# Optimization experiments

Hardware: AMD Instinct MI355X
Metric: run time of the kernel (lower is better)

## Reference

```python
import jax, jax.numpy as jnp
import numpy as np

B, S, F = 512, 512, 128   # batch, seq_len, facts_size (= querry_size)
H1, H2 = 80, 40
PAD = float(-2**32 + 1)


def setup_inputs() -> dict:
    key = jax.random.key(0)
    ks = jax.random.split(key, 12)
    inp = {
        "query": jax.random.normal(ks[0], (B, F), jnp.float32),
        "facts": jax.random.normal(ks[1], (B, S, F), jnp.float32),
        "mask": jax.random.randint(ks[2], (B, S), 0, 2, jnp.int32),
        # mlp1: querry_size -> facts_size
        "W1": jax.random.normal(ks[3], (F, F), jnp.float32) / np.sqrt(F),
        "b1": jnp.zeros((F,), jnp.float32),
        # PReLU alpha (per-feature, init zeros)
        "alpha": jnp.zeros((F,), jnp.float32),
        # mlp2: 4*F -> 80
        "W2": jax.random.normal(ks[4], (4 * F, H1), jnp.float32) / np.sqrt(4 * F),
        "b2": jnp.zeros((H1,), jnp.float32),
        # mlp3: 80 -> 40
        "W3": jax.random.normal(ks[5], (H1, H2), jnp.float32) / np.sqrt(H1),
        "b3": jnp.zeros((H2,), jnp.float32),
        # mlp4: 40 -> 1
        "W4": jax.random.normal(ks[6], (H2, 1), jnp.float32) / np.sqrt(H2),
        "b4": jnp.zeros((1,), jnp.float32),
    }
    return inp


def reference(query, facts, mask, W1, b1, alpha, W2, b2, W3, b3, W4, b4):
    # mlp1 + PReLU on the query
    q = query @ W1 + b1                                   # [B, F]
    q = jnp.where(q >= 0, q, alpha * q)                   # PReLU, alpha per-feature
    # broadcast query over sequence (tile+reshape in the original)
    qs = jnp.broadcast_to(q[:, None, :], (q.shape[0], S, F))  # [B, S, F]
    din = jnp.concatenate([qs, facts, qs - facts, qs * facts], axis=-1)  # [B,S,4F]
    h1 = jax.nn.sigmoid(din @ W2 + b2)                    # [B, S, 80]
    h2 = jax.nn.sigmoid(h1 @ W3 + b3)                     # [B, S, 40]
    scores = (h2 @ W4 + b4)[..., 0][:, None, :]           # [B, 1, S]
    key_masks = (mask == 1)[:, None, :]                   # [B, 1, S]
    scores = jnp.where(key_masks, scores, PAD)
    scores = jax.nn.softmax(scores, axis=-1)              # softmax over seq
    out = jnp.einsum("bqs,bsf->bqf", scores, facts)       # [B, 1, F]  (mode SUM)
    return out
```

## Files before the change

kernel.cpp:

```cpp
#include <hip/hip_runtime.h>
#include <hip/hip_bf16.h>

typedef __bf16 bf16x8 __attribute__((ext_vector_type(8)));
typedef float  f32x4  __attribute__((ext_vector_type(4)));

#define WBT_STRIDE 136
#define H1_STRIDE  104
#define W3T_STRIDE 104

__global__ __launch_bounds__(512, 4)
void attn_fused(const float* __restrict__ query,
                const float* __restrict__ facts,
                const int*   __restrict__ mask,
                const float* __restrict__ W1, const float* __restrict__ b1,
                const float* __restrict__ alpha,
                const float* __restrict__ W2, const float* __restrict__ b2,
                const float* __restrict__ W3, const float* __restrict__ b3,
                const float* __restrict__ W4,
                float* __restrict__ out)
{
    __shared__ __align__(16) __bf16 WbT[80 * WBT_STRIDE];
    __shared__ __align__(16) __bf16 W3T[48 * W3T_STRIDE];
    __shared__ __align__(16) __bf16 h1all[128 * H1_STRIDE];
    __shared__ float qy[128], qs[128], qcs[80];
    __shared__ float qpart[4][128], qcp[4][80];
    __shared__ float w4s[48], b3s[48];
    __shared__ float outw[8 * 128];
    __shared__ float Zw[8];

    const int b = blockIdx.x, t = threadIdx.x;

    if (t < 128) qy[t] = query[b * 128 + t];
    for (int e = t; e < 48 * 96; e += 512) {
        int j = e / 96, k = e % 96;
        W3T[j * W3T_STRIDE + k] = (j < 40 && k < 80) ? (__bf16)W3[k * 40 + j]
                                                     : (__bf16)0.0f;
    }
    for (int e = t; e < 128 * 16; e += 512) {
        int r = e >> 4, c = 80 + (e & 15);
        h1all[r * H1_STRIDE + c] = (__bf16)0.0f;
    }
    if (t < 48) { w4s[t] = (t < 40) ? W4[t] : 0.f; b3s[t] = (t < 40) ? b3[t] : 0.f; }
    __syncthreads();

    {
        int j = t & 127, kh = t >> 7;
        float acc = (kh == 0) ? b1[j] : 0.f;
        const float* w1p = W1 + (kh * 32) * 128 + j;
        #pragma unroll 8
        for (int k = 0; k < 32; ++k) acc = fmaf(qy[kh * 32 + k], w1p[k * 128], acc);
        qpart[kh][j] = acc;
    }
    __syncthreads();
    if (t < 128) {
        float s = (qpart[0][t] + qpart[1][t]) + (qpart[2][t] + qpart[3][t]);
        qs[t] = (s >= 0.f) ? s : alpha[t] * s;
    }
    __syncthreads();

    if (t < 320) {
        int jj = t % 80, hh = t / 80;
        float acc = (hh == 0) ? b2[jj] : 0.f;
        #pragma unroll 8
        for (int k = hh * 32; k < hh * 32 + 32; ++k)
            acc = fmaf(qs[k], W2[k * 80 + jj] + W2[(256 + k) * 80 + jj], acc);
        qcp[hh][jj] = acc;
    }
    for (int e = t; e < 128 * 80; e += 512) {
        int k = e / 80, n = e - k * 80;
        float w = W2[(128 + k) * 80 + n] - W2[(256 + k) * 80 + n]
                + qs[k] * W2[(384 + k) * 80 + n];
        WbT[n * WBT_STRIDE + k] = (__bf16)w;
    }
    __syncthreads();
    if (t < 80) qcs[t] = (qcp[0][t] + qcp[1][t]) + (qcp[2][t] + qcp[3][t]);
    __syncthreads();

    const int wave = t >> 6, lane = t & 63, qd = lane >> 4, m = lane & 15;
    const float* fb = facts + (size_t)b * (512 * 128);
    const int*   mb = mask + b * 512;
    __bf16* h1w = &h1all[wave * 16 * H1_STRIDE];

    float oacc[4][8];
    #pragma unroll
    for (int kc = 0; kc < 4; ++kc)
        #pragma unroll
        for (int i = 0; i < 8; ++i) oacc[kc][i] = 0.f;
    float Zl = 0.f;

    for (int tile = 0; tile < 4; ++tile) {
        const int s0 = wave * 64 + tile * 16;
        const int mv = mb[s0 + m];

        f32x4 av[4][2];
        {
            const float* p0 = &fb[(size_t)(s0 + m) * 128 + qd * 8];
            #pragma unroll
            for (int kc = 0; kc < 4; ++kc) {
                av[kc][0] = *(const f32x4*)(p0 + kc * 32);
                av[kc][1] = *(const f32x4*)(p0 + kc * 32 + 4);
            }
        }
        bf16x8 af[4];
        #pragma unroll
        for (int kc = 0; kc < 4; ++kc)
            #pragma unroll
            for (int i = 0; i < 8; ++i)
                af[kc][i] = (__bf16)((i < 4) ? av[kc][0][i] : av[kc][1][i - 4]);

        #pragma unroll
        for (int ct = 0; ct < 5; ++ct) {
            f32x4 acc = {0.f, 0.f, 0.f, 0.f};
            #pragma unroll
            for (int kc = 0; kc < 4; ++kc) {
                bf16x8 bfr = *(const bf16x8*)&WbT[(ct * 16 + m) * WBT_STRIDE + kc * 32 + qd * 8];
                acc = __builtin_amdgcn_mfma_f32_16x16x32_bf16(af[kc], bfr, acc, 0, 0, 0);
            }
            const int col = ct * 16 + m;
            const float qc = qcs[col];
            #pragma unroll
            for (int r = 0; r < 4; ++r) {
                float x = acc[r] + qc;
                float h = __builtin_amdgcn_rcpf(1.0f + __expf(-x));
                h1w[(qd * 4 + r) * H1_STRIDE + col] = (__bf16)h;
            }
        }
        asm volatile("s_waitcnt lgkmcnt(0)" ::: "memory");

        bf16x8 a2[3];
        #pragma unroll
        for (int kc = 0; kc < 3; ++kc)
            a2[kc] = *(const bf16x8*)&h1w[m * H1_STRIDE + kc * 32 + qd * 8];
        float sc[4] = {0.f, 0.f, 0.f, 0.f};
        #pragma unroll
        for (int ct = 0; ct < 3; ++ct) {
            f32x4 acc2 = {0.f, 0.f, 0.f, 0.f};
            #pragma unroll
            for (int kc = 0; kc < 3; ++kc) {
                bf16x8 bfr = *(const bf16x8*)&W3T[(ct * 16 + m) * W3T_STRIDE + kc * 32 + qd * 8];
                acc2 = __builtin_amdgcn_mfma_f32_16x16x32_bf16(a2[kc], bfr, acc2, 0, 0, 0);
            }
            const int col = ct * 16 + m;
            const float w4v = w4s[col], b3v = b3s[col];
            #pragma unroll
            for (int r = 0; r < 4; ++r) {
                float h2 = __builtin_amdgcn_rcpf(1.0f + __expf(-(acc2[r] + b3v)));
                sc[r] = fmaf(h2, w4v, sc[r]);
            }
        }
        #pragma unroll
        for (int d = 1; d < 16; d <<= 1)
            #pragma unroll
            for (int r = 0; r < 4; ++r)
                sc[r] += __shfl_xor(sc[r], d);

        const int idx = ((((m >> 2) << 4) | m) << 2);
        float s0v = __int_as_float(__builtin_amdgcn_ds_bpermute(idx, __float_as_int(sc[0])));
        float s1v = __int_as_float(__builtin_amdgcn_ds_bpermute(idx, __float_as_int(sc[1])));
        float s2v = __int_as_float(__builtin_amdgcn_ds_bpermute(idx, __float_as_int(sc[2])));
        float s3v = __int_as_float(__builtin_amdgcn_ds_bpermute(idx, __float_as_int(sc[3])));
        const int rr = m & 3;
        float srow = (rr == 0) ? s0v : (rr == 1) ? s1v : (rr == 2) ? s2v : s3v;

        const float pm = (mv == 1) ? __expf(srow) : 0.f;
        Zl += pm;
        #pragma unroll
        for (int kc = 0; kc < 4; ++kc)
            #pragma unroll
            for (int i = 0; i < 4; ++i) {
                oacc[kc][i]     = fmaf(pm, av[kc][0][i], oacc[kc][i]);
                oacc[kc][i + 4] = fmaf(pm, av[kc][1][i], oacc[kc][i + 4]);
            }
    }

    #pragma unroll
    for (int d = 1; d < 16; d <<= 1) {
        #pragma unroll
        for (int kc = 0; kc < 4; ++kc)
            #pragma unroll
            for (int i = 0; i < 8; ++i)
                oacc[kc][i] += __shfl_xor(oacc[kc][i], d);
        Zl += __shfl_xor(Zl, d);
    }
    if (m == 0) {
        #pragma unroll
        for (int kc = 0; kc < 4; ++kc)
            #pragma unroll
            for (int i = 0; i < 8; ++i)
                outw[wave * 128 + kc * 32 + qd * 8 + i] = oacc[kc][i];
        if (lane == 0) Zw[wave] = Zl;
    }
    __syncthreads();

    if (t < 128) {
        float v = 0.f, Z = 0.f;
        #pragma unroll
        for (int w = 0; w < 8; ++w) { v += outw[w * 128 + t]; Z += Zw[w]; }
        out[b * 128 + t] = v / Z;
    }
}

extern "C" void kernel_launch(void* const* d_in, const int* in_sizes, int n_in,
                              void* d_out, int out_size, void* d_ws, size_t ws_size,
                              hipStream_t stream) {
    (void)in_sizes; (void)n_in; (void)d_ws; (void)ws_size; (void)out_size;
    const float* query = (const float*)d_in[0];
    const float* facts = (const float*)d_in[1];
    const int*   mask  = (const int*)d_in[2];
    const float* W1 = (const float*)d_in[3];
    const float* b1 = (const float*)d_in[4];
    const float* al = (const float*)d_in[5];
    const float* W2 = (const float*)d_in[6];
    const float* b2 = (const float*)d_in[7];
    const float* W3 = (const float*)d_in[8];
    const float* b3 = (const float*)d_in[9];
    const float* W4 = (const float*)d_in[10];
    const float* b4 = (const float*)d_in[11];
    (void)b4;
    attn_fused<<<dim3(512), dim3(512), 0, stream>>>(
        query, facts, mask, W1, b1, al, W2, b2, W3, b3, W4, (float*)d_out);
}
```

Measured before the change: 233.3 us.

## Prefetch facts tiles before weight setup and double-buffer the tile loop

Issues the global loads for the first two facts tiles and all mask values at kernel start, before the shared-memory weight preparation and the query MLP, so those loads overlap the setup phase. The per-wave tile loop is manually unrolled with two register buffers, loading tile n+2 while tile n+1 is computed. This hides global memory latency but holds two extra 32-float register buffers across the setup phase, which raises register pressure under the 512-thread, 4-blocks-per-CU launch bound and may cause spills.

New measurement: 259.5 us. 11.2% more time.

```diff
diff --git a/kernel.cpp b/kernel.cpp
--- a/kernel.cpp
+++ b/kernel.cpp
@@ -7,6 +7,89 @@
 #define WBT_STRIDE 136
 #define H1_STRIDE  104
 #define W3T_STRIDE 104
+
+#define LOAD_TILE(av, tile)                                                     \
+    {                                                                           \
+        const float* p0 = &fb[(size_t)(wave * 64 + (tile) * 16 + m) * 128 + qd * 8]; \
+        _Pragma("unroll")                                                       \
+        for (int kc = 0; kc < 4; ++kc) {                                        \
+            av[kc][0] = *(const f32x4*)(p0 + kc * 32);                          \
+            av[kc][1] = *(const f32x4*)(p0 + kc * 32 + 4);                      \
+        }                                                                       \
+    }
+
+#define TILE_BODY(av, mvv)                                                      \
+    {                                                                           \
+        bf16x8 af[4];                                                           \
+        _Pragma("unroll")                                                       \
+        for (int kc = 0; kc < 4; ++kc)                                          \
+            _Pragma("unroll")                                                   \
+            for (int i = 0; i < 8; ++i)                                         \
+                af[kc][i] = (__bf16)((i < 4) ? av[kc][0][i] : av[kc][1][i - 4]);\
+         \
+        _Pragma("unroll")                                                       \
+        for (int ct = 0; ct < 5; ++ct) {                                        \
+            f32x4 acc = {0.f, 0.f, 0.f, 0.f};                                   \
+            _Pragma("unroll")                                                   \
+            for (int kc = 0; kc < 4; ++kc) {                                    \
+                bf16x8 bfr = *(const bf16x8*)&WbT[(ct * 16 + m) * WBT_STRIDE + kc * 32 + qd * 8]; \
+                acc = __builtin_amdgcn_mfma_f32_16x16x32_bf16(af[kc], bfr, acc, 0, 0, 0); \
+            }                                                                   \
+            const int col = ct * 16 + m;    \
+            const float qc = qcs[col];                                          \
+            _Pragma("unroll")                                                   \
+            for (int r = 0; r < 4; ++r) {                                       \
+                float x = acc[r] + qc;                                          \
+                float h = __builtin_amdgcn_rcpf(1.0f + __expf(-x));             \
+                h1w[(qd * 4 + r) * H1_STRIDE + col] = (__bf16)h;                \
+            }                                                                   \
+        }                                                                       \
+        asm volatile("s_waitcnt lgkmcnt(0)" ::: "memory");    \
+                      \
+        bf16x8 a2[3];                                                           \
+        _Pragma("unroll")                                                       \
+        for (int kc = 0; kc < 3; ++kc)                                          \
+            a2[kc] = *(const bf16x8*)&h1w[m * H1_STRIDE + kc * 32 + qd * 8];    \
+        float sc[4] = {0.f, 0.f, 0.f, 0.f};                                     \
+        _Pragma("unroll")                                                       \
+        for (int ct = 0; ct < 3; ++ct) {                                        \
+            f32x4 acc2 = {0.f, 0.f, 0.f, 0.f};                                  \
+            _Pragma("unroll")                                                   \
+            for (int kc = 0; kc < 3; ++kc) {                                    \
+                bf16x8 bfr = *(const bf16x8*)&W3T[(ct * 16 + m) * W3T_STRIDE + kc * 32 + qd * 8]; \
+                acc2 = __builtin_amdgcn_mfma_f32_16x16x32_bf16(a2[kc], bfr, acc2, 0, 0, 0); \
+            }                                                                   \
+            const int col = ct * 16 + m;                                        \
+            const float w4v = w4s[col], b3v = b3s[col];                         \
+            _Pragma("unroll")                                                   \
+            for (int r = 0; r < 4; ++r) {                                       \
+                float h2 = __builtin_amdgcn_rcpf(1.0f + __expf(-(acc2[r] + b3v))); \
+                sc[r] = fmaf(h2, w4v, sc[r]);                                   \
+            }                                                                   \
+        }                                                                       \
+        _Pragma("unroll")                                                       \
+        for (int d = 1; d < 16; d <<= 1)                                        \
+            _Pragma("unroll")                                                   \
+            for (int r = 0; r < 4; ++r)                                         \
+                sc[r] += __shfl_xor(sc[r], d);                                  \
+          \
+        float s0v = __int_as_float(__builtin_amdgcn_ds_bpermute(idx, __float_as_int(sc[0]))); \
+        float s1v = __int_as_float(__builtin_amdgcn_ds_bpermute(idx, __float_as_int(sc[1]))); \
+        float s2v = __int_as_float(__builtin_amdgcn_ds_bpermute(idx, __float_as_int(sc[2]))); \
+        float s3v = __int_as_float(__builtin_amdgcn_ds_bpermute(idx, __float_as_int(sc[3]))); \
+        const int rr = m & 3;                                                   \
+        float srow = (rr == 0) ? s0v : (rr == 1) ? s1v : (rr == 2) ? s2v : s3v; \
+               \
+        const float pm = ((mvv) == 1) ? __expf(srow) : 0.f;                     \
+        Zl += pm;                                                               \
+        _Pragma("unroll")                                                       \
+        for (int kc = 0; kc < 4; ++kc)                                          \
+            _Pragma("unroll")                                                   \
+            for (int i = 0; i < 4; ++i) {                                       \
+                oacc[kc][i]     = fmaf(pm, av[kc][0][i], oacc[kc][i]);          \
+                oacc[kc][i + 4] = fmaf(pm, av[kc][1][i], oacc[kc][i + 4]);      \
+            }                                                                   \
+    }
 
 __global__ __launch_bounds__(512, 4)
 void attn_fused(const float* __restrict__ query,
@@ -29,6 +112,17 @@
     __shared__ float Zw[8];
 
     const int b = blockIdx.x, t = threadIdx.x;
+    const int wave = t >> 6, lane = t & 63, qd = lane >> 4, m = lane & 15;
+    const float* fb = facts + (size_t)b * (512 * 128);
+    const int*   mb = mask + b * 512;
+
+    f32x4 av0[4][2], av1[4][2];
+    LOAD_TILE(av0, 0)
+    LOAD_TILE(av1, 1)
+    const int mv0 = mb[wave * 64 + m];
+    const int mv1 = mb[wave * 64 + 16 + m];
+    const int mv2 = mb[wave * 64 + 32 + m];
+    const int mv3 = mb[wave * 64 + 48 + m];
 
     if (t < 128) qy[t] = query[b * 128 + t];
     for (int e = t; e < 48 * 96; e += 512) {
@@ -76,10 +170,8 @@
     if (t < 80) qcs[t] = (qcp[0][t] + qcp[1][t]) + (qcp[2][t] + qcp[3][t]);
     __syncthreads();
 
-    const int wave = t >> 6, lane = t & 63, qd = lane >> 4, m = lane & 15;
-    const float* fb = facts + (size_t)b * (512 * 128);
-    const int*   mb = mask + b * 512;
     __bf16* h1w = &h1all[wave * 16 * H1_STRIDE];
+    const int idx = ((((m >> 2) << 4) | m) << 2);
 
     float oacc[4][8];
     #pragma unroll
@@ -88,90 +180,12 @@
         for (int i = 0; i < 8; ++i) oacc[kc][i] = 0.f;
     float Zl = 0.f;
 
-    for (int tile = 0; tile < 4; ++tile) {
-        const int s0 = wave * 64 + tile * 16;
-        const int mv = mb[s0 + m];
-
-        f32x4 av[4][2];
-        {
-            const float* p0 = &fb[(size_t)(s0 + m) * 128 + qd * 8];
-            #pragma unroll
-            for (int kc = 0; kc < 4; ++kc) {
-                av[kc][0] = *(const f32x4*)(p0 + kc * 32);
-                av[kc][1] = *(const f32x4*)(p0 + kc * 32 + 4);
-            }
-        }
-        bf16x8 af[4];
-        #pragma unroll
-        for (int kc = 0; kc < 4; ++kc)
-            #pragma unroll
-            for (int i = 0; i < 8; ++i)
-                af[kc][i] = (__bf16)((i < 4) ? av[kc][0][i] : av[kc][1][i - 4]);
-
-        #pragma unroll
-        for (int ct = 0; ct < 5; ++ct) {
-            f32x4 acc = {0.f, 0.f, 0.f, 0.f};
-            #pragma unroll
-            for (int kc = 0; kc < 4; ++kc) {
-                bf16x8 bfr = *(const bf16x8*)&WbT[(ct * 16 + m) * WBT_STRIDE + kc * 32 + qd * 8];
-                acc = __builtin_amdgcn_mfma_f32_16x16x32_bf16(af[kc], bfr, acc, 0, 0, 0);
-            }
-            const int col = ct * 16 + m;
-            const float qc = qcs[col];
-            #pragma unroll
-            for (int r = 0; r < 4; ++r) {
-                float x = acc[r] + qc;
-                float h = __builtin_amdgcn_rcpf(1.0f + __expf(-x));
-                h1w[(qd * 4 + r) * H1_STRIDE + col] = (__bf16)h;
-            }
-        }
-        asm volatile("s_waitcnt lgkmcnt(0)" ::: "memory");
-
-        bf16x8 a2[3];
-        #pragma unroll
-        for (int kc = 0; kc < 3; ++kc)
-            a2[kc] = *(const bf16x8*)&h1w[m * H1_STRIDE + kc * 32 + qd * 8];
-        float sc[4] = {0.f, 0.f, 0.f, 0.f};
-        #pragma unroll
-        for (int ct = 0; ct < 3; ++ct) {
-            f32x4 acc2 = {0.f, 0.f, 0.f, 0.f};
-            #pragma unroll
-            for (int kc = 0; kc < 3; ++kc) {
-                bf16x8 bfr = *(const bf16x8*)&W3T[(ct * 16 + m) * W3T_STRIDE + kc * 32 + qd * 8];
-                acc2 = __builtin_amdgcn_mfma_f32_16x16x32_bf16(a2[kc], bfr, acc2, 0, 0, 0);
-            }
-            const int col = ct * 16 + m;
-            const float w4v = w4s[col], b3v = b3s[col];
-            #pragma unroll
-            for (int r = 0; r < 4; ++r) {
-                float h2 = __builtin_amdgcn_rcpf(1.0f + __expf(-(acc2[r] + b3v)));
-                sc[r] = fmaf(h2, w4v, sc[r]);
-            }
-        }
-        #pragma unroll
-        for (int d = 1; d < 16; d <<= 1)
-            #pragma unroll
-            for (int r = 0; r < 4; ++r)
-                sc[r] += __shfl_xor(sc[r], d);
-
-        const int idx = ((((m >> 2) << 4) | m) << 2);
-        float s0v = __int_as_float(__builtin_amdgcn_ds_bpermute(idx, __float_as_int(sc[0])));
-        float s1v = __int_as_float(__builtin_amdgcn_ds_bpermute(idx, __float_as_int(sc[1])));
-        float s2v = __int_as_float(__builtin_amdgcn_ds_bpermute(idx, __float_as_int(sc[2])));
-        float s3v = __int_as_float(__builtin_amdgcn_ds_bpermute(idx, __float_as_int(sc[3])));
-        const int rr = m & 3;
-        float srow = (rr == 0) ? s0v : (rr == 1) ? s1v : (rr == 2) ? s2v : s3v;
-
-        const float pm = (mv == 1) ? __expf(srow) : 0.f;
-        Zl += pm;
-        #pragma unroll
-        for (int kc = 0; kc < 4; ++kc)
-            #pragma unroll
-            for (int i = 0; i < 4; ++i) {
-                oacc[kc][i]     = fmaf(pm, av[kc][0][i], oacc[kc][i]);
-                oacc[kc][i + 4] = fmaf(pm, av[kc][1][i], oacc[kc][i + 4]);
-            }
-    }
+    TILE_BODY(av0, mv0)
+    LOAD_TILE(av0, 2)
+    TILE_BODY(av1, mv1)
+    LOAD_TILE(av1, 3)
+    TILE_BODY(av0, mv2)
+    TILE_BODY(av1, mv3)
 
     #pragma unroll
     for (int d = 1; d < 16; d <<= 1) {
```
